# Optimization experiments

Measured on AMD Instinct MI355X. Metric: run time of the kernel, lower is better.

The kernel has to match this reference:

```python
import jax, jax.numpy as jnp
import numpy as np
import math

B, N, DIM = 2, 2048, 1024
D_LAYERS, H, DH = 6, 8, 64
INNER = H * DH            # 512
FF_IN = int(DIM * 2 * 4 / 3)  # 2730 (GEGLU inner dim)
NB, MD = 32, 128          # rel-pos buckets / max distance
ALPHA = 0.1               # grad_shrink alpha
EPS = 1e-5


def setup_inputs() -> dict:
    key = jax.random.key(0)
    ks = jax.random.split(key, 8)
    s = 0.02
    return {
        "x": jax.random.normal(ks[0], (B, N, DIM), jnp.float32),
        "rel_emb": jax.random.normal(ks[1], (NB, H), jnp.float32) * s,
        "ln1_g": jnp.ones((D_LAYERS, DIM), jnp.float32),
        "ln1_b": jnp.zeros((D_LAYERS, DIM), jnp.float32),
        "wq": jax.random.normal(ks[2], (D_LAYERS, DIM, INNER), jnp.float32) * s,
        "wkv": jax.random.normal(ks[3], (D_LAYERS, DIM, 2 * DH), jnp.float32) * s,
        "wo": jax.random.normal(ks[4], (D_LAYERS, INNER, DIM), jnp.float32) * s,
        "ln2_g": jnp.ones((D_LAYERS, DIM), jnp.float32),
        "ln2_b": jnp.zeros((D_LAYERS, DIM), jnp.float32),
        "w1": jax.random.normal(ks[5], (D_LAYERS, DIM, 2 * FF_IN), jnp.float32) * s,
        "w2": jax.random.normal(ks[6], (D_LAYERS, FF_IN, DIM), jnp.float32) * s,
        "lnf_g": jnp.ones((DIM,), jnp.float32),
        "lnf_b": jnp.zeros((DIM,), jnp.float32),
    }


def _ln(x, g, b):
    mu = jnp.mean(x, axis=-1, keepdims=True)
    var = jnp.mean(jnp.square(x - mu), axis=-1, keepdims=True)
    return (x - mu) * jax.lax.rsqrt(var + EPS) * g + b


def _rel_pos_bias(rel_emb, n):
    pos = jnp.arange(n)
    rel = pos[None, :] - pos[:, None]        # k_pos - q_pos
    dist = jnp.maximum(-rel, 0)
    max_exact = NB // 2
    is_small = dist < max_exact
    val_large = max_exact + (
        jnp.log(jnp.maximum(dist, 1).astype(jnp.float32) / max_exact)
        / math.log(MD / max_exact) * (NB - max_exact)
    ).astype(jnp.int32)
    val_large = jnp.minimum(val_large, NB - 1)
    bucket = jnp.where(is_small, dist, val_large)
    return jnp.transpose(rel_emb[bucket], (2, 0, 1))  # [H, n, n]


def reference(x, rel_emb, ln1_g, ln1_b, wq, wkv, wo, ln2_g, ln2_b, w1, w2, lnf_g, lnf_b):
    b, n, _ = x.shape
    scale = DH ** -0.5
    # grad_shrink (forward identity, scales gradient by alpha)
    x = x * ALPHA + jax.lax.stop_gradient(x) * (1.0 - ALPHA)
    bias = _rel_pos_bias(rel_emb, n)               # [H, n, n]
    causal = jnp.triu(jnp.ones((n, n), bool), 1)   # mask above diagonal
    neg = -jnp.finfo(x.dtype).max
    for l in range(D_LAYERS):
        # --- causal self-attention (multi-query: shared k/v) ---
        xn = _ln(x, ln1_g[l], ln1_b[l])
        q = (xn @ wq[l]).reshape(b, n, H, DH).transpose(0, 2, 1, 3) * scale  # bhnd
        k, v = jnp.split(xn @ wkv[l], 2, axis=-1)                            # [b,n,DH] each
        sim = jnp.einsum('bhid,bjd->bhij', q, k) + bias[None]
        sim = jnp.where(causal, neg, sim)
        attn = jax.nn.softmax(sim, axis=-1)
        o = jnp.einsum('bhij,bjd->bhid', attn, v).transpose(0, 2, 1, 3).reshape(b, n, INNER)
        x = x + o @ wo[l]
        # --- GEGLU feedforward ---
        xn = _ln(x, ln2_g[l], ln2_b[l])
        h = xn @ w1[l]
        a, g = jnp.split(h, 2, axis=-1)
        x = x + (jax.nn.gelu(g, approximate=False) * a) @ w2[l]
    return _ln(x, lnf_g, lnf_b)
```

## Files before the change

kernel.cpp:

```cpp
#include <hip/hip_runtime.h>
#include <cstdint>
#include <cstddef>

using bf16 = __bf16;
typedef __bf16 bf16x8 __attribute__((ext_vector_type(8)));
typedef __bf16 bf16x4 __attribute__((ext_vector_type(4)));
typedef __bf16 bf16x2 __attribute__((ext_vector_type(2)));
typedef float  f32x4  __attribute__((ext_vector_type(4)));
typedef float  f32x16 __attribute__((ext_vector_type(16)));
typedef int    i32x4  __attribute__((ext_vector_type(4)));
typedef float  f32x4u __attribute__((ext_vector_type(4), aligned(4)));

constexpr int NB   = 2;
constexpr int NN   = 2048;
constexpr int DIM  = 1024;
constexpr int NH   = 8;
constexpr int DH   = 64;
constexpr int INNER= 512;
constexpr int QKVN = 640;
constexpr int FF   = 2730;
constexpr int FFP  = 2816;
constexpr int FF2N = 5632;
constexpr int MROW = NB * NN;
constexpr int NLAY = 6;
constexpr int AROWS = NB * NH * NN;

__device__ __forceinline__ void gload_lds16(const bf16* g, bf16* l) {
  __builtin_amdgcn_global_load_lds((const __attribute__((address_space(1))) void*)g,
                                   (__attribute__((address_space(3))) void*)l,
                                   16, 0, 0);
}

__device__ __forceinline__ int pack_bf16(float lo, float hi_) {
  bf16x2 t; t[0] = (bf16)lo; t[1] = (bf16)hi_;
  return __builtin_bit_cast(int, t);
}

__global__ void btab_kernel(const float* __restrict__ rel, float* __restrict__ btab) {
  int d = blockIdx.x * 256 + threadIdx.x;
  if (d >= NN) return;
  int bucket;
  if (d < 16) bucket = d;
  else {
    int vl = 16 + (int)(logf((float)d / 16.0f) / logf(8.0f) * 16.0f);
    bucket = vl < 31 ? vl : 31;
  }
  for (int h = 0; h < NH; ++h) btab[h * NN + d] = rel[bucket * NH + h];
}

__global__ void conv_tr(const float* __restrict__ src, size_t srcLayer, int srcStride,
                        int colOff, int R, int C,
                        bf16* __restrict__ dst, size_t dstLayer, int Tcols, float scale) {
  __shared__ float tile[32][33];
  const int i0 = blockIdx.x * 32, j0 = blockIdx.y * 32, z = blockIdx.z;
  const float* s = src + (size_t)z * srcLayer;
  bf16* d = dst + (size_t)z * dstLayer;
  const int tx = threadIdx.x, ty = threadIdx.y;
#pragma unroll
  for (int k = 0; k < 4; ++k) {
    int j = j0 + ty + k * 8;
    int i = i0 + tx;
    float v = 0.0f;
    if (j < R && i < C) v = s[(size_t)j * srcStride + colOff + i] * scale;
    tile[ty + k * 8][tx] = v;
  }
  __syncthreads();
#pragma unroll
  for (int k = 0; k < 4; ++k) {
    int i = i0 + ty + k * 8;
    int j = j0 + tx;
    d[(size_t)i * Tcols + j] = (bf16)tile[tx][ty + k * 8];
  }
}

template <typename OUT>
__global__ void ln_kernel(const float* __restrict__ X, const float* __restrict__ G,
                          const float* __restrict__ Bt, OUT* __restrict__ out) {
  __shared__ float red[8];
  const int row = blockIdx.x, t = threadIdx.x;
  const float* xr = X + (size_t)row * DIM;
  float4 v = *(const float4*)(xr + t * 4);
  float s  = v.x + v.y + v.z + v.w;
  float s2 = v.x * v.x + v.y * v.y + v.z * v.z + v.w * v.w;
#pragma unroll
  for (int o = 1; o < 64; o <<= 1) { s += __shfl_xor(s, o); s2 += __shfl_xor(s2, o); }
  if ((t & 63) == 0) { red[t >> 6] = s; red[4 + (t >> 6)] = s2; }
  __syncthreads();
  float S  = red[0] + red[1] + red[2] + red[3];
  float S2 = red[4] + red[5] + red[6] + red[7];
  const float inv = 1.0f / (float)DIM;
  float mu = S * inv;
  float var = S2 * inv - mu * mu;
  float rstd = rsqrtf(var + 1e-5f);
  float4 g  = *(const float4*)(G + t * 4);
  float4 bb = *(const float4*)(Bt + t * 4);
  OUT* orow = out + (size_t)row * DIM + t * 4;
  orow[0] = (OUT)((v.x - mu) * rstd * g.x + bb.x);
  orow[1] = (OUT)((v.y - mu) * rstd * g.y + bb.y);
  orow[2] = (OUT)((v.z - mu) * rstd * g.z + bb.z);
  orow[3] = (OUT)((v.w - mu) * rstd * g.w + bb.w);
}

template <int MODE>
__launch_bounds__(512)
__global__ void gemm_bt(const bf16* __restrict__ A, const bf16* __restrict__ B,
                        int K, int lda, int N, bf16* __restrict__ Cb, float* __restrict__ Xr) {
  __shared__ __align__(16) bf16 As[2][128 * 64];
  __shared__ __align__(16) bf16 Bs[2][128 * 64];
  const int tid = threadIdx.x;
  const int lane = tid & 63, wave = tid >> 6;
  const int gx = gridDim.x, gy = gridDim.y;
  const int nwg = gx * gy;
  const int orig = blockIdx.y * gx + blockIdx.x;
  const int wgid = (orig & 7) * (nwg >> 3) + (orig >> 3);
  const int m0 = (wgid % gy) * 128;
  const int n0 = (wgid / gy) * 128;
  const int wm = (wave >> 2) * 64, wn = (wave & 3) * 32;
  const int fr = lane & 15, fg8 = (lane >> 4) * 8;
  const int frl8 = (fr & 7) * 8;
  const int rL = lane >> 3;
  const int cS = ((lane & 7) ^ rL) * 8;
  const bf16* aB = A + (size_t)(m0 + wave * 8 + rL) * lda + cS;
  const bf16* bB = B + (size_t)(n0 + wave * 8 + rL) * K + cS;
  f32x4 acc[4][2] = {};

  auto STAGE = [&](int buf, int kt) {
#pragma unroll
    for (int r = 0; r < 2; ++r) {
      gload_lds16(aB + (size_t)(r * 64) * lda + kt, &As[buf][(r * 8 + wave) * 512]);
      gload_lds16(bB + (size_t)(r * 64) * K + kt, &Bs[buf][(r * 8 + wave) * 512]);
    }
  };

  STAGE(0, 0);
  const int nt = K >> 6;
  int cur = 0;
  for (int t = 0; t < nt; ++t) {
    asm volatile("s_waitcnt vmcnt(0)" ::: "memory");
    __builtin_amdgcn_s_barrier();
    __builtin_amdgcn_sched_barrier(0);
    if (t + 1 < nt) STAGE(cur ^ 1, (t + 1) * 64);
#pragma unroll
    for (int kk = 0; kk < 64; kk += 32) {
      bf16x8 af[4], bfr[2];
#pragma unroll
      for (int m = 0; m < 4; ++m)
        af[m] = *(const bf16x8*)&As[cur][(wm + m * 16 + fr) * 64 + ((kk + fg8) ^ frl8)];
#pragma unroll
      for (int n = 0; n < 2; ++n)
        bfr[n] = *(const bf16x8*)&Bs[cur][(wn + n * 16 + fr) * 64 + ((kk + fg8) ^ frl8)];
#pragma unroll
      for (int m = 0; m < 4; ++m)
#pragma unroll
        for (int n = 0; n < 2; ++n)
          acc[m][n] = __builtin_amdgcn_mfma_f32_16x16x32_bf16(af[m], bfr[n], acc[m][n], 0, 0, 0);
    }
    __builtin_amdgcn_sched_barrier(0);
    cur ^= 1;
  }
  const int cc = lane & 15, cg = (lane >> 4) * 4;
#pragma unroll
  for (int m = 0; m < 4; ++m) {
#pragma unroll
    for (int n = 0; n < 2; ++n) {
      const int col = n0 + wn + n * 16 + cc;
#pragma unroll
      for (int r = 0; r < 4; ++r) {
        const int row = m0 + wm + m * 16 + cg + r;
        const size_t idx = (size_t)row * N + col;
        if (MODE == 0) Cb[idx] = (bf16)acc[m][n][r];
        else           Xr[idx] += acc[m][n][r];
      }
    }
  }
}

__global__ void vt_kernel(const bf16* __restrict__ QKV, bf16* __restrict__ VT) {
  __shared__ bf16 t[32][33];
  const int n0 = blockIdx.x * 32, d0 = blockIdx.y * 32, b = blockIdx.z;
  const int tx = threadIdx.x, ty = threadIdx.y;
#pragma unroll
  for (int k = 0; k < 4; ++k) {
    int n = n0 + ty + k * 8;
    t[ty + k * 8][tx] = QKV[(size_t)(b * NN + n) * QKVN + 576 + d0 + tx];
  }
  __syncthreads();
#pragma unroll
  for (int k = 0; k < 4; ++k) {
    int dh = d0 + ty + k * 8;
    VT[(size_t)(b * 64 + dh) * NN + n0 + tx] = t[tx][ty + k * 8];
  }
}

__launch_bounds__(256)
__global__ void attn_kernel(const bf16* __restrict__ QKV, const bf16* __restrict__ VT,
                            const float* __restrict__ btab,
                            float* __restrict__ Opart, float* __restrict__ mlbuf) {
  const int tid = threadIdx.x;
  const int lane = tid & 63, wv = tid >> 6;
  const int split = blockIdx.x & 1;
  const int qt = (NN / 32 - 1) - (blockIdx.x >> 1);
  const int h = blockIdx.y * 4 + wv, b = blockIdx.z;
  const int q0 = qt * 32;
  const int qc = lane & 31;
  const int hid = lane >> 5;
  const int h8 = hid * 8;
  const int kv_full = q0 + 32;
  const int half = (kv_full > 32) ? ((kv_full / 2) & ~31) : 0;
  const int lo = split ? half : 0;
  const int kend = split ? kv_full : half;
  const size_t obase = ((size_t)split * NB * NH + b * NH + h) * 64;
  const int Rbase = (b * NH + h) * NN + q0;
  if (kend <= lo) {
#pragma unroll
    for (int dd = 0; dd < 32; ++dd)
      Opart[(obase + dd * 2 + hid) * NN + q0 + qc] = 0.0f;
    if (hid == 0)
      ((float2*)mlbuf)[(size_t)split * AROWS + Rbase + qc] = make_float2(-1e30f, 0.0f);
    return;
  }
  const float* bt = btab + h * NN;
  bf16x8 qf[4];
#pragma unroll
  for (int ks = 0; ks < 4; ++ks)
    qf[ks] = *(const bf16x8*)&QKV[(size_t)(b * NN + q0 + qc) * QKVN + h * DH + ks * 16 + h8];

  f32x16 Oacc0 = {}, Oacc1 = {};
  float m_run = -1e30f, l_run = 0.0f;
  int kv0 = lo;

  while (kv0 < kend) {
    const bool interior = (kv0 + 32 <= q0);
    bf16x8 kf[4];
#pragma unroll
    for (int ks = 0; ks < 4; ++ks)
      kf[ks] = *(const bf16x8*)&QKV[(size_t)(b * NN + kv0 + qc) * QKVN + 512 + ks * 16 + h8];
    bf16x8 vf[2][2];
#pragma unroll
    for (int dblk = 0; dblk < 2; ++dblk)
#pragma unroll
      for (int ks2 = 0; ks2 < 2; ++ks2)
        vf[dblk][ks2] = *(const bf16x8*)&VT[(size_t)(b * 64 + dblk * 32 + qc) * NN + kv0 + ks2 * 16 + h8];
    __builtin_amdgcn_s_setprio(1);
    f32x16 S = {};
#pragma unroll
    for (int ks = 0; ks < 4; ++ks)
      S = __builtin_amdgcn_mfma_f32_32x32x16_bf16(kf[ks], qf[ks], S, 0, 0, 0);
    __builtin_amdgcn_s_setprio(0);
    float sv[16];
    float mx = -1e30f;
    if (interior) {
      f32x4 bv[4];
#pragma unroll
      for (int g = 0; g < 4; ++g)
        bv[g] = *(const f32x4u*)(bt + (q0 + qc - kv0 - 8 * g - 4 * hid - 3));
#pragma unroll
      for (int g = 0; g < 4; ++g)
#pragma unroll
        for (int e = 0; e < 4; ++e) {
          const float val = S[g * 4 + e] + bv[g][3 - e];
          sv[g * 4 + e] = val;
          mx = fmaxf(mx, val);
        }
    } else {
#pragma unroll
      for (int r = 0; r < 16; ++r) {
        const int kvr = (r & 3) + 8 * (r >> 2) + 4 * hid;
        const int d = (q0 + qc) - (kv0 + kvr);
        const int dc = d > 0 ? d : 0;
        float val = S[r] + bt[dc];
        if (d < 0) val = -1e30f;
        sv[r] = val;
        mx = fmaxf(mx, val);
      }
    }
    if (!__all(mx <= m_run + 8.0f)) {
      mx = fmaxf(mx, __shfl_xor(mx, 32));
      const float m_new = fmaxf(m_run, mx);
      const float sc = __expf(m_run - m_new);
      l_run *= sc;
#pragma unroll
      for (int r = 0; r < 16; ++r) { Oacc0[r] *= sc; Oacc1[r] *= sc; }
      m_run = m_new;
    }
    float csum = 0.0f;
#pragma unroll
    for (int r = 0; r < 16; ++r) { sv[r] = __expf(sv[r] - m_run); csum += sv[r]; }
    csum += __shfl_xor(csum, 32);
    l_run += csum;
    int w[8];
#pragma unroll
    for (int g = 0; g < 4; ++g) {
      w[2 * g]     = pack_bf16(sv[4 * g],     sv[4 * g + 1]);
      w[2 * g + 1] = pack_bf16(sv[4 * g + 2], sv[4 * g + 3]);
    }
    bf16x8 pfrag[2];
#pragma unroll
    for (int ks2 = 0; ks2 < 2; ++ks2) {
      const int a  = w[4 * ks2],     bb = w[4 * ks2 + 1];
      const int c  = w[4 * ks2 + 2], dd = w[4 * ks2 + 3];
      const int s0 = hid ? a : c,    s1 = hid ? bb : dd;
      const int r0 = __shfl_xor(s0, 32);
      const int r1 = __shfl_xor(s1, 32);
      i32x4 fw;
      fw[0] = hid ? r0 : a;
      fw[1] = hid ? r1 : bb;
      fw[2] = hid ? c  : r0;
      fw[3] = hid ? dd : r1;
      pfrag[ks2] = __builtin_bit_cast(bf16x8, fw);
    }
    __builtin_amdgcn_s_setprio(1);
#pragma unroll
    for (int ks2 = 0; ks2 < 2; ++ks2) {
      Oacc0 = __builtin_amdgcn_mfma_f32_32x32x16_bf16(vf[0][ks2], pfrag[ks2], Oacc0, 0, 0, 0);
      Oacc1 = __builtin_amdgcn_mfma_f32_32x32x16_bf16(vf[1][ks2], pfrag[ks2], Oacc1, 0, 0, 0);
    }
    __builtin_amdgcn_s_setprio(0);
    kv0 += 32;
  }
#pragma unroll
  for (int r = 0; r < 16; ++r) {
    const int dl = (r & 3) + 8 * (r >> 2) + 4 * hid;
    Opart[(obase + dl) * NN + q0 + qc]      = Oacc0[r];
    Opart[(obase + 32 + dl) * NN + q0 + qc] = Oacc1[r];
  }
  if (hid == 0)
    ((float2*)mlbuf)[(size_t)split * AROWS + Rbase + qc] = make_float2(m_run, l_run);
}

__global__ void attn_combine(const float* __restrict__ Opart, const float* __restrict__ mlbuf,
                             bf16* __restrict__ O) {
  const int gtid = blockIdx.x * 256 + threadIdx.x;
  const int q  = gtid & (NN - 1);
  const int dq = (gtid >> 11) & 15;
  const int bh = gtid >> 15;
  const int R = bh * NN + q;
  const float2 ml0 = ((const float2*)mlbuf)[R];
  const float2 ml1 = ((const float2*)mlbuf)[AROWS + R];
  const float m = fmaxf(ml0.x, ml1.x);
  const float w0 = __expf(ml0.x - m), w1 = __expf(ml1.x - m);
  const float inv = 1.0f / (ml0.y * w0 + ml1.y * w1);
  const size_t r0 = ((size_t)bh * 64 + dq * 4) * NN + q;
  const size_t r1 = ((size_t)(NB * NH + bh) * 64 + dq * 4) * NN + q;
  bf16x4 res;
#pragma unroll
  for (int j = 0; j < 4; ++j)
    res[j] = (bf16)((Opart[r0 + j * NN] * w0 + Opart[r1 + j * NN] * w1) * inv);
  const int h = bh & (NH - 1), b = bh >> 3;
  *(bf16x4*)&O[(size_t)(b * NN + q) * INNER + h * DH + dq * 4] = res;
}

__global__ void gelu_mul_kernel(bf16* __restrict__ h) {
  const size_t total = (size_t)MROW * FFP / 8;
  for (size_t i = (size_t)blockIdx.x * blockDim.x + threadIdx.x; i < total;
       i += (size_t)gridDim.x * blockDim.x) {
    const size_t row = i / (FFP / 8), c8 = i % (FFP / 8);
    bf16* base = h + row * FF2N + c8 * 8;
    bf16x8 a = *(const bf16x8*)base;
    bf16x8 g = *(const bf16x8*)(base + FFP);
    bf16x8 r;
#pragma unroll
    for (int j = 0; j < 8; ++j) {
      float gv = (float)g[j], av = (float)a[j];
      float ge = 0.5f * gv * (1.0f + erff(gv * 0.70710678118654752f));
      r[j] = (bf16)(ge * av);
    }
    *(bf16x8*)base = r;
  }
}

extern "C" void kernel_launch(void* const* d_in, const int* in_sizes, int n_in,
                              void* d_out, int out_size, void* d_ws, size_t ws_size,
                              hipStream_t stream) {
  (void)in_sizes; (void)n_in; (void)out_size;
  const float* in_x  = (const float*)d_in[0];
  const float* rel   = (const float*)d_in[1];
  const float* ln1g  = (const float*)d_in[2];
  const float* ln1b  = (const float*)d_in[3];
  const float* wq    = (const float*)d_in[4];
  const float* wkv   = (const float*)d_in[5];
  const float* wo    = (const float*)d_in[6];
  const float* ln2g  = (const float*)d_in[7];
  const float* ln2b  = (const float*)d_in[8];
  const float* w1    = (const float*)d_in[9];
  const float* w2    = (const float*)d_in[10];
  const float* lnfg  = (const float*)d_in[11];
  const float* lnfb  = (const float*)d_in[12];
  float* out = (float*)d_out;

  constexpr size_t E_QKV = (size_t)QKVN * DIM;
  constexpr size_t E_WO  = (size_t)DIM * INNER;
  constexpr size_t E_W1F = (size_t)FF2N * DIM;
  constexpr size_t E_W2  = (size_t)DIM * FFP;
  bf16* wqkvT = (bf16*)d_ws;
  bf16* woT  = wqkvT + NLAY * E_QKV;
  bf16* w1fT = woT  + NLAY * E_WO;
  bf16* w2T  = w1fT + NLAY * E_W1F;
  bf16* xnb  = w2T  + NLAY * E_W2;
  bf16* qkvb = xnb  + (size_t)MROW * DIM;
  bf16* vTb  = qkvb + (size_t)MROW * QKVN;
  bf16* ob   = vTb  + (size_t)NB * 64 * NN;
  bf16* hb   = ob   + (size_t)MROW * INNER;
  float* xbuf = (float*)(hb + (size_t)MROW * FF2N);
  float* btab = xbuf + (size_t)MROW * DIM;
  const size_t needed = (size_t)((char*)(btab + NH * NN) - (char*)d_ws);
  if (ws_size < needed) return;
  float* Opart = (float*)hb;
  float* mlbuf = (float*)(hb + (size_t)19 * 1024 * 1024);
  hipMemcpyAsync(xbuf, in_x, (size_t)MROW * DIM * sizeof(float),
                 hipMemcpyDeviceToDevice, stream);
  btab_kernel<<<8, 256, 0, stream>>>(rel, btab);

  const dim3 tb(32, 8);
  conv_tr<<<dim3(16, 32, 6), tb, 0, stream>>>(wq,  (size_t)DIM*INNER, INNER, 0, DIM, INNER,
                                              wqkvT, E_QKV, DIM, 0.125f);
  conv_tr<<<dim3(4, 32, 6),  tb, 0, stream>>>(wkv, (size_t)DIM*128, 128, 0, DIM, 128,
                                              wqkvT + (size_t)INNER*DIM, E_QKV, DIM, 1.0f);
  conv_tr<<<dim3(32, 16, 6), tb, 0, stream>>>(wo,  (size_t)INNER*DIM, DIM, 0, INNER, DIM,
                                              woT,  E_WO, INNER, 1.0f);
  conv_tr<<<dim3(88, 32, 6), tb, 0, stream>>>(w1,  (size_t)DIM*2*FF, 2*FF, 0, DIM, FF,
                                              w1fT, E_W1F, DIM, 1.0f);
  conv_tr<<<dim3(88, 32, 6), tb, 0, stream>>>(w1,  (size_t)DIM*2*FF, 2*FF, FF, DIM, FF,
                                              w1fT + (size_t)FFP*DIM, E_W1F, DIM, 1.0f);
  conv_tr<<<dim3(32, 88, 6), tb, 0, stream>>>(w2,  (size_t)FF*DIM, DIM, 0, FF, DIM,
                                              w2T,  E_W2, FFP, 1.0f);

  for (int l = 0; l < NLAY; ++l) {
    ln_kernel<bf16><<<MROW, 256, 0, stream>>>(xbuf, ln1g + l*DIM, ln1b + l*DIM, xnb);
    gemm_bt<0><<<dim3(QKVN/128, MROW/128), 512, 0, stream>>>(xnb, wqkvT + l*E_QKV, DIM, DIM, QKVN, qkvb, nullptr);
    vt_kernel<<<dim3(NN/32, 2, NB), tb, 0, stream>>>(qkvb, vTb);
    attn_kernel<<<dim3((NN/32)*2, NH/4, NB), 256, 0, stream>>>(qkvb, vTb, btab, Opart, mlbuf);
    attn_combine<<<AROWS*16/256, 256, 0, stream>>>(Opart, mlbuf, ob);
    gemm_bt<1><<<dim3(DIM/128, MROW/128), 512, 0, stream>>>(ob, woT + l*E_WO, INNER, INNER, DIM, nullptr, xbuf);
    ln_kernel<bf16><<<MROW, 256, 0, stream>>>(xbuf, ln2g + l*DIM, ln2b + l*DIM, xnb);
    gemm_bt<0><<<dim3(FF2N/128, MROW/128), 512, 0, stream>>>(xnb, w1fT + l*E_W1F, DIM, DIM, FF2N, hb, nullptr);
    gelu_mul_kernel<<<2048, 256, 0, stream>>>(hb);
    gemm_bt<1><<<dim3(DIM/128, MROW/128), 512, 0, stream>>>(hb, w2T + l*E_W2, FFP, FF2N, DIM, nullptr, xbuf);
  }
  ln_kernel<float><<<MROW, 256, 0, stream>>>(xbuf, lnfg, lnfb, out);
}
```

Before: 1.797 ms.

## Add 256x256-tile double-buffered GEMM for the GEGLU up-projection

Adds a dedicated 256x256 output-tile bf16 MFMA GEMM with double-buffered direct-to-LDS loads, XOR-swizzled LDS layout, workgroup-id remapping, and interleaved prefetch of the next K tile between MFMA phases. It replaces the 128x128 generic GEMM only for the largest per-layer GEMM (xn @ w1, N=5632). The larger tile raises arithmetic intensity and cuts global/LDS traffic per FLOP. The cost is high register and LDS usage (128 KB LDS), and with only 22x16=352 workgroups the grid may map unevenly onto the CUs.

Result: slower. 1.925 ms (+7.1%).

```diff
diff --git a/kernel.cpp b/kernel.cpp
--- a/kernel.cpp
+++ b/kernel.cpp
@@ -175,6 +175,89 @@
   }
 }
 
+__launch_bounds__(512, 2)
+__global__ void gemm256(const bf16* __restrict__ A, const bf16* __restrict__ B,
+                        const int K, const int N, bf16* __restrict__ Cb) {
+  __shared__ __align__(16) bf16 As[2][256 * 64];
+  __shared__ __align__(16) bf16 Bs[2][256 * 64];
+  const int tid = threadIdx.x;
+  const int lane = tid & 63, wave = tid >> 6;
+  const int gx = gridDim.x, gy = gridDim.y;
+  const int nwg = gx * gy;
+  const int orig = blockIdx.y * gx + blockIdx.x;
+  const int wgid = (orig & 7) * (nwg >> 3) + (orig >> 3);
+  const int m0 = (wgid % gy) * 256;
+  const int n0 = (wgid / gy) * 256;
+  const int wm = (wave >> 2) * 128, wn = (wave & 3) * 64;
+  const int fr = lane & 15, fg8 = (lane >> 4) * 8;
+  const int frl8 = (fr & 7) * 8;
+  const int rL = lane >> 3;
+  const int cS = ((lane & 7) ^ rL) * 8;
+  const bf16* aB = A + (size_t)(m0 + wave * 8 + rL) * K + cS;
+  const bf16* bB = B + (size_t)(n0 + wave * 8 + rL) * K + cS;
+  f32x4 acc[8][4] = {};
+
+  auto CHUNK = [&](int buf, int kt, int r) {
+    gload_lds16(aB + (size_t)(r * 64) * K + kt, &As[buf][(r * 64 + wave * 8) * 64]);
+    gload_lds16(bB + (size_t)(r * 64) * K + kt, &Bs[buf][(r * 64 + wave * 8) * 64]);
+  };
+#pragma unroll
+  for (int r = 0; r < 4; ++r) CHUNK(0, 0, r);
+
+  const int nt = K >> 6;
+  for (int t = 0; t < nt; ++t) {
+    const int cur = t & 1, nxt = cur ^ 1;
+    const bool more = (t + 1 < nt);
+    __builtin_amdgcn_s_barrier();
+    if (more) {
+      CHUNK(nxt, (t + 1) * 64, 0);
+      asm volatile("s_waitcnt vmcnt(2)" ::: "memory");
+    } else {
+      asm volatile("s_waitcnt vmcnt(0)" ::: "memory");
+    }
+    __builtin_amdgcn_s_barrier();
+#pragma unroll
+    for (int p = 0; p < 4; ++p) {
+      if (p && more) CHUNK(nxt, (t + 1) * 64, p);
+      const int mh = (p >> 1) * 4, nh = (p & 1) * 2;
+      bf16x8 af[4][2], bfr[2][2];
+#pragma unroll
+      for (int mi = 0; mi < 4; ++mi)
+#pragma unroll
+        for (int kkI = 0; kkI < 2; ++kkI)
+          af[mi][kkI] = *(const bf16x8*)&As[cur][(wm + (mh + mi) * 16 + fr) * 64 + ((kkI * 32 + fg8) ^ frl8)];
+#pragma unroll
+      for (int ni = 0; ni < 2; ++ni)
+#pragma unroll
+        for (int kkI = 0; kkI < 2; ++kkI)
+          bfr[ni][kkI] = *(const bf16x8*)&Bs[cur][(wn + (nh + ni) * 16 + fr) * 64 + ((kkI * 32 + fg8) ^ frl8)];
+      __builtin_amdgcn_s_setprio(1);
+#pragma unroll
+      for (int kkI = 0; kkI < 2; ++kkI)
+#pragma unroll
+        for (int mi = 0; mi < 4; ++mi)
+#pragma unroll
+          for (int ni = 0; ni < 2; ++ni)
+            acc[mh + mi][nh + ni] = __builtin_amdgcn_mfma_f32_16x16x32_bf16(
+                af[mi][kkI], bfr[ni][kkI], acc[mh + mi][nh + ni], 0, 0, 0);
+      __builtin_amdgcn_s_setprio(0);
+      __builtin_amdgcn_sched_barrier(0);
+    }
+  }
+  const int cc = lane & 15, cg = (lane >> 4) * 4;
+#pragma unroll
+  for (int m = 0; m < 8; ++m)
+#pragma unroll
+    for (int n = 0; n < 4; ++n) {
+      const int col = n0 + wn + n * 16 + cc;
+#pragma unroll
+      for (int r = 0; r < 4; ++r) {
+        const int row = m0 + wm + m * 16 + cg + r;
+        Cb[(size_t)row * N + col] = (bf16)acc[m][n][r];
+      }
+    }
+}
+
 __global__ void vt_kernel(const bf16* __restrict__ QKV, bf16* __restrict__ VT) {
   __shared__ bf16 t[32][33];
   const int n0 = blockIdx.x * 32, d0 = blockIdx.y * 32, b = blockIdx.z;
@@ -433,7 +516,7 @@
     attn_combine<<<AROWS*16/256, 256, 0, stream>>>(Opart, mlbuf, ob);
     gemm_bt<1><<<dim3(DIM/128, MROW/128), 512, 0, stream>>>(ob, woT + l*E_WO, INNER, INNER, DIM, nullptr, xbuf);
     ln_kernel<bf16><<<MROW, 256, 0, stream>>>(xbuf, ln2g + l*DIM, ln2b + l*DIM, xnb);
-    gemm_bt<0><<<dim3(FF2N/128, MROW/128), 512, 0, stream>>>(xnb, w1fT + l*E_W1F, DIM, DIM, FF2N, hb, nullptr);
+    gemm256<<<dim3(FF2N/256, MROW/256), 512, 0, stream>>>(xnb, w1fT + l*E_W1F, DIM, FF2N, hb);
     gelu_mul_kernel<<<2048, 256, 0, stream>>>(hb);
     gemm_bt<1><<<dim3(DIM/128, MROW/128), 512, 0, stream>>>(hb, w2T + l*E_W2, FFP, FF2N, DIM, nullptr, xbuf);
   }
```
